# Kernel optimization log

Hardware: AMD Instinct MI355X
Metric: run time of the kernel (lower is better)

The kernel has to match this reference:

```python
import jax, jax.numpy as jnp
import numpy as np

B, C, H, W = 8, 256, 32, 32
N_HEAD, D_K, D_V, OUT_C = 8, 32, 32, 256


def _relative_indices(height, width):
    # idx[i, j] = (y_j - y_i + H) * W + (x_j - x_i + W), matching the torch loop
    ys, xs = np.meshgrid(np.arange(height), np.arange(width), indexing='ij')
    ys, xs = ys.reshape(-1), xs.reshape(-1)  # [L]
    rel_y = ys[None, :] - ys[:, None] + height  # [L, L]
    rel_x = xs[None, :] - xs[:, None] + width
    return jnp.asarray(rel_y * width + rel_x, dtype=jnp.int32)


def setup_inputs() -> dict:
    key = jax.random.key(0)
    ks = jax.random.split(key, 7)
    sc = lambda fan_in: 1.0 / np.sqrt(fan_in)
    table = ((2 * H - 1) * (2 * W - 1))  # 3969
    return {
        'x': jax.random.normal(ks[0], (B, C, H, W), jnp.float32),
        'Qw': jax.random.normal(ks[1], (C, N_HEAD * D_K), jnp.float32) * sc(C),
        'Kw': jax.random.normal(ks[2], (C, N_HEAD * D_K), jnp.float32) * sc(C),
        'Vw': jax.random.normal(ks[3], (C, N_HEAD * D_V), jnp.float32) * sc(C),
        'ffw': jax.random.normal(ks[4], (N_HEAD * D_V, OUT_C), jnp.float32) * sc(N_HEAD * D_V),
        'ffb': jax.random.normal(ks[5], (OUT_C,), jnp.float32) * 0.01,
        'rel_bias': jax.random.normal(ks[6], (N_HEAD, table), jnp.float32),
        'rel_idx': _relative_indices(H, W),  # [L, L] int32
    }


def reference(x, Qw, Kw, Vw, ffw, ffb, rel_bias, rel_idx):
    b, c, h_, w_ = x.shape
    L = h_ * w_
    nh = rel_bias.shape[0]
    dk = Qw.shape[1] // nh
    dv = Vw.shape[1] // nh
    xf = x.reshape(b, c, L).transpose(0, 2, 1)  # [b, L, c]
    q = (xf @ Qw).reshape(b, L, nh, dk).transpose(0, 2, 1, 3)  # [b, h, L, dk]
    k = (xf @ Kw).reshape(b, L, nh, dk).transpose(0, 2, 1, 3)
    v = (xf @ Vw).reshape(b, L, nh, dv).transpose(0, 2, 1, 3)
    bias = rel_bias[:, rel_idx]  # gather -> [h, L, L]
    sim = jnp.einsum('bhid,bhjd->bhij', q, k) + bias[None]  # no 1/sqrt(dk) in original
    attn = jax.nn.softmax(sim, axis=-1)  # dropout is identity in eval
    out = jnp.einsum('bhij,bhjd->bhid', attn, v)  # [b, h, L, dv]
    out = out.transpose(0, 2, 1, 3).reshape(b, L, nh * dv)
    out = out @ ffw + ffb  # [b, L, out_c]
    return out.transpose(0, 2, 1).reshape(b, -1, h_, w_)
```

## Files before the change

kernel.cpp:

```cpp
#include <hip/hip_runtime.h>
#include <math.h>


typedef unsigned short u16;
typedef __bf16 bf16;
typedef bf16 bf16x8 __attribute__((ext_vector_type(8)));
typedef bf16 bf16x4 __attribute__((ext_vector_type(4)));
typedef short s16x4 __attribute__((ext_vector_type(4)));
typedef float f32x4 __attribute__((ext_vector_type(4)));
typedef float f32x4u __attribute__((ext_vector_type(4), aligned(4)));
typedef u16 u16x8 __attribute__((ext_vector_type(8)));
typedef u16 u16x4 __attribute__((ext_vector_type(4)));

#define DEVI __device__ __forceinline__

DEVI u16 bfbits(float f) { return __builtin_bit_cast(u16, (bf16)f); }

DEVI void async_cp16(const u16* g, u16* l) {
    __builtin_amdgcn_global_load_lds((const __attribute__((address_space(1))) void*)g,
                                     (__attribute__((address_space(3))) void*)l, 16, 0, 0);
}

DEVI f32x4 pv_mfma(bf16x4 a, bf16x4 b, f32x4 c) {
#if __has_builtin(__builtin_amdgcn_mfma_f32_16x16x16bf16_1k)
    return __builtin_amdgcn_mfma_f32_16x16x16bf16_1k(
        __builtin_bit_cast(s16x4, a), __builtin_bit_cast(s16x4, b), c, 0, 0, 0);
#else
    asm("s_nop 1\n\tv_mfma_f32_16x16x16_bf16 %0, %1, %2, %0"
        : "+v"(c) : "v"(a), "v"(b));
    return c;
#endif
}

__global__ __launch_bounds__(256) void prep(const float* __restrict__ X,
                                            const float* __restrict__ Qw, const float* __restrict__ Kw,
                                            const float* __restrict__ Vw, const float* __restrict__ Fw,
                                            const float* __restrict__ RB,
                                            u16* __restrict__ XF, u16* __restrict__ WT,
                                            float* __restrict__ RBs) {
    __shared__ u16 t[64 * 65];
    const int blk = blockIdx.x, tid = threadIdx.x;
    if (blk < 576) {
        const float* src;
        int cbase, rbase, rows_total;
        u16* dst;
        if (blk < 512) {
            const int b = blk >> 6;
            cbase = (blk & 3) * 64; rbase = ((blk >> 2) & 15) * 64;
            src = X + (size_t)b * 256 * 1024; dst = XF + (size_t)b * 1024 * 256;
            rows_total = 1024;
        } else {
            const int t2 = blk - 512, wsel = t2 >> 4;
            cbase = (t2 & 3) * 64; rbase = ((t2 >> 2) & 3) * 64;
            src = wsel == 0 ? Qw : wsel == 1 ? Kw : wsel == 2 ? Vw : Fw;
            dst = WT + (size_t)wsel * 256 * 256;
            rows_total = 256;
        }
        const int w = tid >> 6, r = tid & 63;
#pragma unroll
        for (int i = 0; i < 16; i++) {
            const int c = w * 16 + i;
            t[c * 65 + r] = bfbits(src[(size_t)(cbase + c) * rows_total + rbase + r]);
        }
        __syncthreads();
#pragma unroll
        for (int i = 0; i < 2; i++) {
            const int idx = i * 256 + tid;
            const int r2 = idx >> 3, cg = idx & 7;
            u16x8 v;
#pragma unroll
            for (int j = 0; j < 8; j++) v[j] = t[(cg * 8 + j) * 65 + r2];
            *(u16x8*)&dst[(size_t)(rbase + r2) * 256 + cbase + cg * 8] = v;
        }
    } else {
        const int n = 8 * 3969;
        for (int i = (blk - 576) * 256 + tid; i < n; i += 32 * 256)
            RBs[i] = RB[i] * 1.44269504f;
    }
}

__global__ __launch_bounds__(256, 6) void gemm_fused(const u16* __restrict__ xf, const u16* __restrict__ wt,
                                                     u16* __restrict__ q, u16* __restrict__ kk,
                                                     u16* __restrict__ vt, const u16* __restrict__ ob,
                                                     float* __restrict__ outf, const float* __restrict__ ffb,
                                                     int base_mode) {
    __shared__ __align__(16) u16 lA[64 * 32];
    __shared__ __align__(16) u16 lB[64 * 32];
    const int tid = threadIdx.x;
    const int wave = tid >> 6, lane = tid & 63;
    const int quad = lane >> 4, l15 = lane & 15;

    int mode, mbase, nbase;
    const u16 *A, *Bt;
    if (base_mode == 2) {
        mode = 2; A = wt + 768 * 256; Bt = ob;
        mbase = (blockIdx.x & 3) * 64; nbase = (blockIdx.x >> 2) * 64;
    } else if (blockIdx.x < 1024) {
        mode = 0; A = xf; Bt = wt;
        mbase = (blockIdx.x >> 3) * 64; nbase = (blockIdx.x & 7) * 64;
    } else {
        mode = 1; A = wt + 512 * 256; Bt = xf;
        const int t = blockIdx.x - 1024;
        mbase = (t & 3) * 64; nbase = (t >> 2) * 64;
    }

    const int m0 = (wave >> 1) * 32, n0 = (wave & 1) * 32;
    const int srow = tid >> 2;
    const int k8 = (tid & 3) * 8;

    f32x4 acc[2][2];
#pragma unroll
    for (int i = 0; i < 2; i++)
#pragma unroll
        for (int j = 0; j < 2; j++) acc[i][j] = f32x4{0.f, 0.f, 0.f, 0.f};

    for (int kb = 0; kb < 256; kb += 32) {
        __syncthreads();
        *(u16x8*)&lA[srow * 32 + k8] = *(const u16x8*)&A[(size_t)(mbase + srow) * 256 + kb + k8];
        *(u16x8*)&lB[srow * 32 + k8] = *(const u16x8*)&Bt[(size_t)(nbase + srow) * 256 + kb + k8];
        __syncthreads();
        bf16x8 af[2], bfr[2];
#pragma unroll
        for (int i = 0; i < 2; i++) af[i] = *(const bf16x8*)&lA[(m0 + i * 16 + l15) * 32 + quad * 8];
#pragma unroll
        for (int j = 0; j < 2; j++) bfr[j] = *(const bf16x8*)&lB[(n0 + j * 16 + l15) * 32 + quad * 8];
#pragma unroll
        for (int i = 0; i < 2; i++)
#pragma unroll
            for (int j = 0; j < 2; j++)
                acc[i][j] = __builtin_amdgcn_mfma_f32_16x16x32_bf16(af[i], bfr[j], acc[i][j], 0, 0, 0);
    }

#pragma unroll
    for (int i = 0; i < 2; i++) {
#pragma unroll
        for (int j = 0; j < 2; j++) {
#pragma unroll
            for (int r = 0; r < 4; r++) {
                const int gm = mbase + m0 + i * 16 + quad * 4 + r;
                const int gn = nbase + n0 + j * 16 + l15;
                float v = acc[i][j][r];
                if (mode == 0) {
                    const int b = gm >> 10, l = gm & 1023;
                    int n = gn;
                    u16* dst = q;
                    if (n >= 256) { n -= 256; dst = kk; }
                    else v *= 1.44269504f;
                    const int h = n >> 5, d = n & 31;
                    dst[(((size_t)(b * 8 + h) * 1024 + l) << 5) + d] = bfbits(v);
                } else if (mode == 1) {
                    const int h = gm >> 5, d = gm & 31;
                    const int b = gn >> 10, l = gn & 1023;
                    vt[(((size_t)(b * 8 + h) * 32 + d) << 10) + l] = bfbits(v);
                } else {
                    const int b = gn >> 10, l = gn & 1023;
                    outf[(((size_t)(b * 256 + gm)) << 10) + l] = v + ffb[gm];
                }
            }
        }
    }
}

__global__ __launch_bounds__(256, 4) void attn(const u16* __restrict__ Q, const u16* __restrict__ Kb,
                                               const u16* __restrict__ Vt, const float* __restrict__ RBs,
                                               u16* __restrict__ O) {
    __shared__ __align__(16) u16 kbuf[2][32 * 32];
    __shared__ __align__(16) u16 vbuf[2][32 * 32];
    const int tid = threadIdx.x;
    const int wave = tid >> 6, lane = tid & 63;
    const int quad = lane >> 4, l15 = lane & 15;
    const int blk = blockIdx.x;
    const int bh = ((blk >> 7) << 3) + (blk & 7);
    const int qt = (blk >> 3) & 15;
    const int b = bh >> 3, h = bh & 7;
    const int qbase = qt * 64 + wave * 16;
    const size_t bhL = (size_t)bh * 1024;

    const bf16x8 qf = *(const bf16x8*)&Q[(bhL + qbase + l15) * 32 + quad * 8];
    const float* brow0 = RBs + (size_t)h * 3969
                         + (32 - (qbase >> 5)) * 32 + 32 - (qbase & 31) - l15 + quad * 4;
    const int srow = lane >> 2;
    const int sgcol = (lane & 3) ^ ((lane >> 3) & 3);
    const u16* ksrc = &Kb[bhL * 32];
    const u16* vsrc_lo = &Vt[(((size_t)bh * 32) + srow) << 10];
    const u16* vsrc_hi = &Vt[(((size_t)bh * 32) + 16 + srow) << 10];

    float lsum = 0.f;
    f32x4 o_lo{0.f, 0.f, 0.f, 0.f}, o_hi{0.f, 0.f, 0.f, 0.f};

#define STAGE(buf, c) do {                                                       \
        const int kb_ = (c) * 32;                                                \
        async_cp16(ksrc + kb_ * 32 + srow * 32 + sgcol * 8, &kbuf[buf][0]);      \
        async_cp16(ksrc + kb_ * 32 + 512 + srow * 32 + sgcol * 8, &kbuf[buf][512]); \
        async_cp16(vsrc_lo + kb_ + sgcol * 8, &vbuf[buf][0]);                    \
        async_cp16(vsrc_hi + kb_ + sgcol * 8, &vbuf[buf][512]);                  \
    } while (0)

    if (wave == 0) STAGE(0, 0);
    __syncthreads();

    const int swz = (l15 >> 1) & 3;
    const int kcol = (quad ^ swz) * 8;
    const int g0 = (2 * ((quad >> 1) ^ swz) + (quad & 1)) * 4;
    const int g1 = (2 * (((quad >> 1) + 2) ^ swz) + (quad & 1)) * 4;

    for (int c = 0; c < 32; c++) {
        const int cur = c & 1;
        if (wave == 0 && c < 31) STAGE(cur ^ 1, c + 1);
        const bf16x8 kf0 = *(const bf16x8*)&kbuf[cur][l15 * 32 + kcol];
        const bf16x8 kf1 = *(const bf16x8*)&kbuf[cur][(16 + l15) * 32 + kcol];
        const bf16x4 v00 = __builtin_bit_cast(bf16x4, *(const u16x4*)&vbuf[cur][l15 * 32 + g0]);
        const bf16x4 v10 = __builtin_bit_cast(bf16x4, *(const u16x4*)&vbuf[cur][l15 * 32 + g1]);
        const bf16x4 v01 = __builtin_bit_cast(bf16x4, *(const u16x4*)&vbuf[cur][(16 + l15) * 32 + g0]);
        const bf16x4 v11 = __builtin_bit_cast(bf16x4, *(const u16x4*)&vbuf[cur][(16 + l15) * 32 + g1]);
        const f32x4u b0 = *(const f32x4u*)(brow0 + c * 32);
        const f32x4u b1 = *(const f32x4u*)(brow0 + c * 32 + 16);
        const f32x4 z{0.f, 0.f, 0.f, 0.f};
        f32x4 s0 = __builtin_amdgcn_mfma_f32_16x16x32_bf16(kf0, qf, z, 0, 0, 0);
        f32x4 s1 = __builtin_amdgcn_mfma_f32_16x16x32_bf16(kf1, qf, z, 0, 0, 0);
        bf16x4 p0, p1;
#pragma unroll
        for (int r = 0; r < 4; r++) {
            const float e0 = exp2f(s0[r] + b0[r]);
            const float e1 = exp2f(s1[r] + b1[r]);
            lsum += e0 + e1;
            p0[r] = (bf16)e0;
            p1[r] = (bf16)e1;
        }
        o_lo = pv_mfma(p0, v00, o_lo);
        o_hi = pv_mfma(p0, v01, o_hi);
        o_lo = pv_mfma(p1, v10, o_lo);
        o_hi = pv_mfma(p1, v11, o_hi);
        __syncthreads();
    }
#undef STAGE
    lsum += __shfl_xor(lsum, 16);
    lsum += __shfl_xor(lsum, 32);
#pragma unroll
    for (int r = 0; r < 4; r++) {
        const float inv = 1.f / __shfl(lsum, quad * 4 + r);
        const int i = qbase + quad * 4 + r;
        O[((size_t)(b * 1024 + i) * 256) + h * 32 + l15] = bfbits(o_lo[r] * inv);
        O[((size_t)(b * 1024 + i) * 256) + h * 32 + 16 + l15] = bfbits(o_hi[r] * inv);
    }
}

extern "C" void kernel_launch(void* const* d_in, const int* in_sizes, int n_in,
                              void* d_out, int out_size, void* d_ws, size_t ws_size,
                              hipStream_t stream) {
    const float* x   = (const float*)d_in[0];
    const float* Qw  = (const float*)d_in[1];
    const float* Kw  = (const float*)d_in[2];
    const float* Vw  = (const float*)d_in[3];
    const float* Fw  = (const float*)d_in[4];
    const float* ffb = (const float*)d_in[5];
    const float* RB  = (const float*)d_in[6];

    u16* ws = (u16*)d_ws;
    u16* xf = ws;
    u16* wt = xf + 2097152;
    u16* q  = wt + 262144;
    u16* kk = q  + 2097152;
    u16* vt = kk + 2097152;
    float* RBs = (float*)(vt + 2097152);
    u16* ob = xf;

    prep<<<dim3(608), 256, 0, stream>>>(x, Qw, Kw, Vw, Fw, RB, xf, wt, RBs);
    gemm_fused<<<dim3(1536), 256, 0, stream>>>(xf, wt, q, kk, vt, nullptr, nullptr, nullptr, 0);
    attn<<<dim3(1024), 256, 0, stream>>>(q, kk, vt, RBs, ob);
    gemm_fused<<<dim3(512), 256, 0, stream>>>(xf, wt, q, kk, vt, ob, (float*)d_out, ffb, 2);
}
```

Measured before the change: 130.0 us.

## Give each attention wave private K/V buffers and drop block barriers; async-load GEMM tiles

In the attention kernel each wave now stages its own double-buffered copy of the K/V chunk into private LDS and waits with s_waitcnt vmcnt instead of block-wide __syncthreads, so waves no longer stall on each other. This quadruples LDS use per block and repeats the global K/V reads four times per block. The GEMM kernel switches its tile staging to direct global-to-LDS async copies with a swizzled column layout to avoid bank conflicts. Relying on vmcnt ordering without a barrier assumes each wave reads only the LDS it wrote itself.

Result: no change. 131.0 us (+0.8%).

```diff
diff --git a/kernel.cpp b/kernel.cpp
--- a/kernel.cpp
+++ b/kernel.cpp
@@ -106,7 +106,10 @@
 
     const int m0 = (wave >> 1) * 32, n0 = (wave & 1) * 32;
     const int srow = tid >> 2;
-    const int k8 = (tid & 3) * 8;
+    const int sgcol = (lane & 3) ^ ((lane >> 3) & 3);
+    const size_t arow = (size_t)(mbase + srow) * 256 + sgcol * 8;
+    const size_t brow = (size_t)(nbase + srow) * 256 + sgcol * 8;
+    const int kcol = ((quad ^ ((l15 >> 1) & 3))) * 8;
 
     f32x4 acc[2][2];
 #pragma unroll
@@ -116,14 +119,14 @@
 
     for (int kb = 0; kb < 256; kb += 32) {
         __syncthreads();
-        *(u16x8*)&lA[srow * 32 + k8] = *(const u16x8*)&A[(size_t)(mbase + srow) * 256 + kb + k8];
-        *(u16x8*)&lB[srow * 32 + k8] = *(const u16x8*)&Bt[(size_t)(nbase + srow) * 256 + kb + k8];
+        async_cp16(&A[arow + kb], &lA[wave * 512]);
+        async_cp16(&Bt[brow + kb], &lB[wave * 512]);
         __syncthreads();
         bf16x8 af[2], bfr[2];
 #pragma unroll
-        for (int i = 0; i < 2; i++) af[i] = *(const bf16x8*)&lA[(m0 + i * 16 + l15) * 32 + quad * 8];
-#pragma unroll
-        for (int j = 0; j < 2; j++) bfr[j] = *(const bf16x8*)&lB[(n0 + j * 16 + l15) * 32 + quad * 8];
+        for (int i = 0; i < 2; i++) af[i] = *(const bf16x8*)&lA[(m0 + i * 16 + l15) * 32 + kcol];
+#pragma unroll
+        for (int j = 0; j < 2; j++) bfr[j] = *(const bf16x8*)&lB[(n0 + j * 16 + l15) * 32 + kcol];
 #pragma unroll
         for (int i = 0; i < 2; i++)
 #pragma unroll
@@ -164,8 +167,8 @@
 __global__ __launch_bounds__(256, 4) void attn(const u16* __restrict__ Q, const u16* __restrict__ Kb,
                                                const u16* __restrict__ Vt, const float* __restrict__ RBs,
                                                u16* __restrict__ O) {
-    __shared__ __align__(16) u16 kbuf[2][32 * 32];
-    __shared__ __align__(16) u16 vbuf[2][32 * 32];
+    __shared__ __align__(16) u16 kbuf[4][2][32 * 32];
+    __shared__ __align__(16) u16 vbuf[4][2][32 * 32];
     const int tid = threadIdx.x;
     const int wave = tid >> 6, lane = tid & 63;
     const int quad = lane >> 4, l15 = lane & 15;
@@ -188,52 +191,57 @@
     float lsum = 0.f;
     f32x4 o_lo{0.f, 0.f, 0.f, 0.f}, o_hi{0.f, 0.f, 0.f, 0.f};
 
-#define STAGE(buf, c) do {                                                       \
-        const int kb_ = (c) * 32;                                                \
-        async_cp16(ksrc + kb_ * 32 + srow * 32 + sgcol * 8, &kbuf[buf][0]);      \
-        async_cp16(ksrc + kb_ * 32 + 512 + srow * 32 + sgcol * 8, &kbuf[buf][512]); \
-        async_cp16(vsrc_lo + kb_ + sgcol * 8, &vbuf[buf][0]);                    \
-        async_cp16(vsrc_hi + kb_ + sgcol * 8, &vbuf[buf][512]);                  \
-    } while (0)
-
-    if (wave == 0) STAGE(0, 0);
-    __syncthreads();
-
     const int swz = (l15 >> 1) & 3;
     const int kcol = (quad ^ swz) * 8;
     const int g0 = (2 * ((quad >> 1) ^ swz) + (quad & 1)) * 4;
     const int g1 = (2 * (((quad >> 1) + 2) ^ swz) + (quad & 1)) * 4;
 
-    for (int c = 0; c < 32; c++) {
-        const int cur = c & 1;
-        if (wave == 0 && c < 31) STAGE(cur ^ 1, c + 1);
-        const bf16x8 kf0 = *(const bf16x8*)&kbuf[cur][l15 * 32 + kcol];
-        const bf16x8 kf1 = *(const bf16x8*)&kbuf[cur][(16 + l15) * 32 + kcol];
-        const bf16x4 v00 = __builtin_bit_cast(bf16x4, *(const u16x4*)&vbuf[cur][l15 * 32 + g0]);
-        const bf16x4 v10 = __builtin_bit_cast(bf16x4, *(const u16x4*)&vbuf[cur][l15 * 32 + g1]);
-        const bf16x4 v01 = __builtin_bit_cast(bf16x4, *(const u16x4*)&vbuf[cur][(16 + l15) * 32 + g0]);
-        const bf16x4 v11 = __builtin_bit_cast(bf16x4, *(const u16x4*)&vbuf[cur][(16 + l15) * 32 + g1]);
-        const f32x4u b0 = *(const f32x4u*)(brow0 + c * 32);
-        const f32x4u b1 = *(const f32x4u*)(brow0 + c * 32 + 16);
-        const f32x4 z{0.f, 0.f, 0.f, 0.f};
-        f32x4 s0 = __builtin_amdgcn_mfma_f32_16x16x32_bf16(kf0, qf, z, 0, 0, 0);
-        f32x4 s1 = __builtin_amdgcn_mfma_f32_16x16x32_bf16(kf1, qf, z, 0, 0, 0);
-        bf16x4 p0, p1;
-#pragma unroll
-        for (int r = 0; r < 4; r++) {
-            const float e0 = exp2f(s0[r] + b0[r]);
-            const float e1 = exp2f(s1[r] + b1[r]);
-            lsum += e0 + e1;
-            p0[r] = (bf16)e0;
-            p1[r] = (bf16)e1;
-        }
-        o_lo = pv_mfma(p0, v00, o_lo);
-        o_hi = pv_mfma(p0, v01, o_hi);
-        o_lo = pv_mfma(p1, v10, o_lo);
-        o_hi = pv_mfma(p1, v11, o_hi);
-        __syncthreads();
-    }
+#define STAGE(buf, c) do {                                                              \
+        const int kb_ = (c) * 32;                                                       \
+        async_cp16(ksrc + kb_ * 32 + srow * 32 + sgcol * 8, &kbuf[wave][buf][0]);       \
+        async_cp16(ksrc + kb_ * 32 + 512 + srow * 32 + sgcol * 8, &kbuf[wave][buf][512]); \
+        async_cp16(vsrc_lo + kb_ + sgcol * 8, &vbuf[wave][buf][0]);                     \
+        async_cp16(vsrc_hi + kb_ + sgcol * 8, &vbuf[wave][buf][512]);                   \
+    } while (0)
+
+#define COMPUTE(cur, c) do {                                                              \
+        const bf16x8 kf0 = *(const bf16x8*)&kbuf[wave][cur][l15 * 32 + kcol];             \
+        const bf16x8 kf1 = *(const bf16x8*)&kbuf[wave][cur][(16 + l15) * 32 + kcol];      \
+        const bf16x4 v00 = __builtin_bit_cast(bf16x4, *(const u16x4*)&vbuf[wave][cur][l15 * 32 + g0]); \
+        const bf16x4 v10 = __builtin_bit_cast(bf16x4, *(const u16x4*)&vbuf[wave][cur][l15 * 32 + g1]); \
+        const bf16x4 v01 = __builtin_bit_cast(bf16x4, *(const u16x4*)&vbuf[wave][cur][(16 + l15) * 32 + g0]); \
+        const bf16x4 v11 = __builtin_bit_cast(bf16x4, *(const u16x4*)&vbuf[wave][cur][(16 + l15) * 32 + g1]); \
+        const f32x4u b0 = *(const f32x4u*)(brow0 + (c) * 32);                             \
+        const f32x4u b1 = *(const f32x4u*)(brow0 + (c) * 32 + 16);                        \
+        const f32x4 z{0.f, 0.f, 0.f, 0.f};                                                \
+        f32x4 s0 = __builtin_amdgcn_mfma_f32_16x16x32_bf16(kf0, qf, z, 0, 0, 0);          \
+        f32x4 s1 = __builtin_amdgcn_mfma_f32_16x16x32_bf16(kf1, qf, z, 0, 0, 0);          \
+        bf16x4 p0, p1;                                                                    \
+        _Pragma("unroll")                                                                 \
+        for (int r = 0; r < 4; r++) {                                                     \
+            const float e0 = exp2f(s0[r] + b0[r]);                                        \
+            const float e1 = exp2f(s1[r] + b1[r]);                                        \
+            lsum += e0 + e1;                                                              \
+            p0[r] = (bf16)e0;                                                             \
+            p1[r] = (bf16)e1;                                                             \
+        }                                                                                 \
+        o_lo = pv_mfma(p0, v00, o_lo);                                                    \
+        o_hi = pv_mfma(p0, v01, o_hi);                                                    \
+        o_lo = pv_mfma(p1, v10, o_lo);                                                    \
+        o_hi = pv_mfma(p1, v11, o_hi);                                                    \
+    } while (0)
+
+    STAGE(0, 0);
+    for (int c = 0; c < 31; c++) {
+        STAGE((c + 1) & 1, c + 1);
+        asm volatile("s_waitcnt vmcnt(4)" ::: "memory");
+        COMPUTE(c & 1, c);
+    }
+    asm volatile("s_waitcnt vmcnt(0)" ::: "memory");
+    COMPUTE(1, 31);
 #undef STAGE
+#undef COMPUTE
+
     lsum += __shfl_xor(lsum, 16);
     lsum += __shfl_xor(lsum, 32);
 #pragma unroll
```
